# Kernel optimization log

Hardware: AMD Instinct MI355X
Metric: run time of the kernel (lower is better)

## Reference

```python
import jax, jax.numpy as jnp
import numpy as np

C, HEADS, H, W = 256, 8, 64, 64
HD = C // HEADS
EPS = 1e-5

def conv1x1(x, w, b):
    # x:[B,C,H,W], w:[O,C], b:[O]
    return jnp.einsum('bchw,oc->bohw', x, w) + b[None, :, None, None]

def group_norm(x, scale, bias):
    B = x.shape[0]
    xg = x.reshape(B, HEADS, HD, H, W)
    mu = jnp.mean(xg, axis=(2, 3, 4), keepdims=True)
    var = jnp.var(xg, axis=(2, 3, 4), keepdims=True)
    xn = ((xg - mu) * jax.lax.rsqrt(var + EPS)).reshape(B, C, H, W)
    return xn * scale[None, :, None, None] + bias[None, :, None, None]

def setup_inputs() -> dict:
    key = jax.random.key(0)
    ks = jax.random.split(key, 12)
    s = 1.0 / np.sqrt(C)
    d = {
        'x': jax.random.normal(ks[0], (1, C, H, W), jnp.float32),
        'wq': jax.random.normal(ks[1], (C, C), jnp.float32) * s,
        'bq': jax.random.normal(ks[2], (C,), jnp.float32) * 0.01,
        'wk': jax.random.normal(ks[3], (C, C), jnp.float32) * s,
        'bk': jax.random.normal(ks[4], (C,), jnp.float32) * 0.01,
        'wv': jax.random.normal(ks[5], (C, C), jnp.float32) * s,
        'bv': jax.random.normal(ks[6], (C,), jnp.float32) * 0.01,
        'wo': jax.random.normal(ks[7], (C, C), jnp.float32) * s,
        'bo': jax.random.normal(ks[8], (C,), jnp.float32) * 0.01,
        'gn_scale': jnp.ones((C,), jnp.float32),
        'gn_bias': jnp.zeros((C,), jnp.float32),
        'gamma': jax.random.normal(ks[9], (1,), jnp.float32) * 0.1,
    }
    return d

def reference(x, wq, bq, wk, bk, wv, bv, wo, bo, gn_scale, gn_bias, gamma):
    B = x.shape[0]
    N = H * W
    scale = HD ** (-0.5)
    xn = group_norm(x, gn_scale, gn_bias)
    q = conv1x1(xn, wq, bq).reshape(B, HEADS, HD, N)
    k = conv1x1(xn, wk, bk).reshape(B, HEADS, HD, N)
    v = conv1x1(xn, wv, bv).reshape(B, HEADS, HD, N)
    attn = jnp.einsum('bhdn,bhdm->bhnm', q, k) * scale  # [B,h,N,N]
    attn = jax.nn.softmax(attn, axis=-1)
    out = jnp.einsum('bhnm,bhdm->bhdn', attn, v).reshape(B, C, H, W)
    out = conv1x1(out, wo, bo)
    return x + gamma * out
```

## Files before the change

kernel.cpp:

```cpp
#include <hip/hip_runtime.h>
#include <hip/hip_bf16.h>

#define C_DIM 256
#define N_SP  4096
#define HEADS 8
#define HD    32
#define GSIZE (HD * N_SP)

typedef __attribute__((ext_vector_type(8))) short bf16x8;
typedef __attribute__((ext_vector_type(4))) float f32x4;
typedef __attribute__((ext_vector_type(4))) unsigned u32x4;

__device__ inline unsigned short f2bf(float f) {
  unsigned int u = __builtin_bit_cast(unsigned int, f);
  u = (u + 0x7fffu + ((u >> 16) & 1u)) >> 16;
  return (unsigned short)u;
}
__device__ inline float bf2f(unsigned short b) {
  return __builtin_bit_cast(float, (unsigned)b << 16);
}

__device__ inline unsigned cvtpk_bf16(float lo, float hi) {
  unsigned r;
  asm("v_cvt_pk_bf16_f32 %0, %1, %2" : "=v"(r) : "v"(lo), "v"(hi));
  return r;
}
__device__ inline void pl32swap(unsigned &x, unsigned &y) {
  asm("v_permlane32_swap_b32 %0, %1" : "+v"(x), "+v"(y));
}
__device__ inline void pl16swap(unsigned &x, unsigned &y) {
  asm("v_permlane16_swap_b32 %0, %1" : "+v"(x), "+v"(y));
}
__device__ inline void gload_lds16(const void* g, void* l) {
  __builtin_amdgcn_global_load_lds(
      (const __attribute__((address_space(1))) void*)g,
      (__attribute__((address_space(3))) void*)l, 16, 0, 0);
}

__global__ __launch_bounds__(1024) void stats_cvt(const float* __restrict__ x,
                                                  float* __restrict__ pstats,
                                                  const float* __restrict__ wq,
                                                  const float* __restrict__ wk,
                                                  const float* __restrict__ wv,
                                                  const float* __restrict__ wo,
                                                  unsigned short* __restrict__ dst) {
  int t = threadIdx.x;
  if (blockIdx.x < 64) {
    int g = blockIdx.x >> 3, sub = blockIdx.x & 7;
    const float4* xg = reinterpret_cast<const float4*>(
        x + (size_t)g * GSIZE + (size_t)sub * (GSIZE / 8));
    float s1 = 0.f, s2 = 0.f;
#pragma unroll
    for (int i = 0; i < 4; ++i) {
      float4 v = xg[t + i * 1024];
      s1 += v.x + v.y + v.z + v.w;
      s2 += v.x * v.x + v.y * v.y + v.z * v.z + v.w * v.w;
    }
    for (int off = 1; off < 64; off <<= 1) {
      s1 += __shfl_xor(s1, off);
      s2 += __shfl_xor(s2, off);
    }
    __shared__ float red[16][2];
    int wid = t >> 6;
    if ((t & 63) == 0) { red[wid][0] = s1; red[wid][1] = s2; }
    __syncthreads();
    if (t < 16) {
      s1 = red[t][0]; s2 = red[t][1];
      for (int off = 1; off < 16; off <<= 1) {
        s1 += __shfl_xor(s1, off);
        s2 += __shfl_xor(s2, off);
      }
      if (t == 0) {
        pstats[(g * 8 + sub) * 2] = s1;
        pstats[(g * 8 + sub) * 2 + 1] = s2;
      }
    }
  } else {
    int i = (blockIdx.x - 64) * 1024 + t;
    int mat = i >> 14;
    int idx = i & 16383;
    const float* src = (mat == 0) ? wq : (mat == 1) ? wk : (mat == 2) ? wv : wo;
    float4 v = reinterpret_cast<const float4*>(src)[idx];
    ushort4 o;
    o.x = f2bf(v.x); o.y = f2bf(v.y); o.z = f2bf(v.z); o.w = f2bf(v.w);
    reinterpret_cast<ushort4*>(dst + (size_t)mat * 65536)[idx] = o;
  }
}

__global__ __launch_bounds__(256) void gn_qkv(const float* __restrict__ x,
                                              const float* __restrict__ pstats,
                                              const float* __restrict__ gsc,
                                              const float* __restrict__ gbi,
                                              const unsigned short* __restrict__ wbf,
                                              const float* __restrict__ bq,
                                              const float* __restrict__ bk,
                                              const float* __restrict__ bv,
                                              unsigned short* __restrict__ qt,
                                              unsigned short* __restrict__ kt,
                                              unsigned short* __restrict__ vv) {
  __shared__ unsigned short xt[16][264];
  int t = threadIdx.x;
  int p0 = (blockIdx.x >> 1) * 16;
  int oh = (blockIdx.x & 1) * 128;

  {
    int pl = t & 15;
    int cb = t >> 4;
    int c0 = cb * 16;
    int g = c0 >> 5;
    float s1 = 0.f, s2 = 0.f;
#pragma unroll
    for (int s = 0; s < 8; ++s) {
      s1 += pstats[(g * 8 + s) * 2];
      s2 += pstats[(g * 8 + s) * 2 + 1];
    }
    float mu = s1 / (float)GSIZE;
    float rs = rsqrtf(s2 / (float)GSIZE - mu * mu + 1e-5f);
#pragma unroll
    for (int j = 0; j < 16; ++j) {
      float sc = gsc[c0 + j] * rs;
      float bi = gbi[c0 + j] - mu * sc;
      xt[pl][c0 + j] = f2bf(x[(size_t)(c0 + j) * N_SP + p0 + pl] * sc + bi);
    }
  }
  __syncthreads();

  int w = t >> 6, lc = t & 15, lg = (t & 63) >> 4;
  int ow = oh + w * 32;
  f32x4 aq[2], ak[2], av[2];
#pragma unroll
  for (int i = 0; i < 2; ++i) {
    aq[i] = (f32x4){0.f, 0.f, 0.f, 0.f};
    ak[i] = (f32x4){0.f, 0.f, 0.f, 0.f};
    av[i] = (f32x4){0.f, 0.f, 0.f, 0.f};
  }
#pragma unroll
  for (int it = 0; it < 8; ++it) {
    bf16x8 a = *reinterpret_cast<const bf16x8*>(&xt[lc][it * 32 + 8 * lg]);
#pragma unroll
    for (int ni = 0; ni < 2; ++ni) {
      size_t rowoff = (size_t)(ow + 16 * ni + lc) * C_DIM + it * 32 + 8 * lg;
      bf16x8 bQ = *reinterpret_cast<const bf16x8*>(wbf + rowoff);
      bf16x8 bK = *reinterpret_cast<const bf16x8*>(wbf + 65536 + rowoff);
      bf16x8 bV = *reinterpret_cast<const bf16x8*>(wbf + 131072 + rowoff);
      aq[ni] = __builtin_amdgcn_mfma_f32_16x16x32_bf16(a, bQ, aq[ni], 0, 0, 0);
      ak[ni] = __builtin_amdgcn_mfma_f32_16x16x32_bf16(a, bK, ak[ni], 0, 0, 0);
      av[ni] = __builtin_amdgcn_mfma_f32_16x16x32_bf16(bV, a, av[ni], 0, 0, 0);
    }
  }
#pragma unroll
  for (int ni = 0; ni < 2; ++ni) {
    int o = ow + 16 * ni + lc;
    float bqv = bq[o], bkv = bk[o];
#pragma unroll
    for (int r = 0; r < 4; ++r) {
      qt[(size_t)(p0 + 4 * lg + r) * C_DIM + o] =
          f2bf((aq[ni][r] + bqv) * 0.25503344494963116f);
      kt[(size_t)(p0 + 4 * lg + r) * C_DIM + o] = f2bf(ak[ni][r] + bkv);
    }
  }
#pragma unroll
  for (int mi = 0; mi < 2; ++mi)
#pragma unroll
    for (int r = 0; r < 4; ++r) {
      int o = ow + 16 * mi + 4 * lg + r;
      vv[(size_t)o * N_SP + p0 + lc] = f2bf(av[mi][r] + bv[o]);
    }
}


#define STAGE_Q(BB, IT)                                                       \
  {                                                                           \
    _Pragma("unroll")                                                         \
    for (int st = 0; st < 4; ++st) {                                          \
      gload_lds16(ksrc + (size_t)(IT) * 131072 + st * 32768,                  \
                  smem + (BB) + st * 4096 + w1024);                           \
      gload_lds16(vsrc + (size_t)(IT) * 512 + st * 128,                       \
                  smem + (BB) + 16384 + st * 4096 + w1024);                   \
    }                                                                         \
  }

#define CHAIN(KF, VF)                                                         \
  {                                                                           \
    f32x4 s[4];                                                               \
    _Pragma("unroll")                                                         \
    for (int ni = 0; ni < 4; ++ni) {                                          \
      f32x4 z = (f32x4){0.f, 0.f, 0.f, 0.f};                                  \
      s[ni] = __builtin_amdgcn_mfma_f32_16x16x32_bf16(KF[ni], qf[qi], z, 0, 0, 0); \
    }                                                                         \
    unsigned wd[4][2];                                                        \
    _Pragma("unroll")                                                         \
    for (int ni = 0; ni < 4; ++ni) {                                          \
      float p0e = __builtin_amdgcn_exp2f(s[ni][0]);                           \
      float p1e = __builtin_amdgcn_exp2f(s[ni][1]);                           \
      float p2e = __builtin_amdgcn_exp2f(s[ni][2]);                           \
      float p3e = __builtin_amdgcn_exp2f(s[ni][3]);                           \
      wd[ni][0] = cvtpk_bf16(p0e, p1e);                                       \
      wd[ni][1] = cvtpk_bf16(p2e, p3e);                                       \
    }                                                                         \
    bf16x8 ap[2];                                                             \
    _Pragma("unroll")                                                         \
    for (int kk = 0; kk < 2; ++kk) {                                          \
      unsigned a0 = wd[2 * kk][0], b0 = wd[2 * kk + 1][0];                    \
      unsigned a1 = wd[2 * kk][1], b1 = wd[2 * kk + 1][1];                    \
      pl32swap(a0, b0); pl16swap(a0, b0);                                     \
      pl32swap(a1, b1); pl16swap(a1, b1);                                     \
      u32x4 pk = {a0, a1, b0, b1};                                            \
      ap[kk] = __builtin_bit_cast(bf16x8, pk);                                \
    }                                                                         \
    lacc[qi] = __builtin_amdgcn_mfma_f32_16x16x32_bf16(ap[0], ones, lacc[qi], 0, 0, 0); \
    oacc[qi][0] = __builtin_amdgcn_mfma_f32_16x16x32_bf16(ap[0], VF[0][0], oacc[qi][0], 0, 0, 0); \
    oacc[qi][1] = __builtin_amdgcn_mfma_f32_16x16x32_bf16(ap[0], VF[0][1], oacc[qi][1], 0, 0, 0); \
    lacc[qi] = __builtin_amdgcn_mfma_f32_16x16x32_bf16(ap[1], ones, lacc[qi], 0, 0, 0); \
    oacc[qi][0] = __builtin_amdgcn_mfma_f32_16x16x32_bf16(ap[1], VF[1][0], oacc[qi][0], 0, 0, 0); \
    oacc[qi][1] = __builtin_amdgcn_mfma_f32_16x16x32_bf16(ap[1], VF[1][1], oacc[qi][1], 0, 0, 0); \
  }

#define COMPUTE_PAIR(BB, KOFF)                                                \
  {                                                                           \
    bf16x8 kf0[4], kf1[4], vf0[2][2], vf1[2][2];                              \
    _Pragma("unroll")                                                         \
    for (int ni = 0; ni < 4; ++ni) {                                          \
      kf0[ni] = *reinterpret_cast<const bf16x8*>(smem + (BB) + (KOFF) + ni * 1024 + krd); \
      kf1[ni] = *reinterpret_cast<const bf16x8*>(smem + (BB) + (KOFF) + 4096 + ni * 1024 + krd); \
    }                                                                         \
    _Pragma("unroll")                                                         \
    for (int dd = 0; dd < 2; ++dd) {                                          \
      vf0[0][dd] = *reinterpret_cast<const bf16x8*>(smem + (BB) + 16384 + (KOFF) + dd * 2048 + vrd0); \
      vf0[1][dd] = *reinterpret_cast<const bf16x8*>(smem + (BB) + 16384 + (KOFF) + dd * 2048 + vrd1); \
      vf1[0][dd] = *reinterpret_cast<const bf16x8*>(smem + (BB) + 16384 + (KOFF) + 4096 + dd * 2048 + vrd0); \
      vf1[1][dd] = *reinterpret_cast<const bf16x8*>(smem + (BB) + 16384 + (KOFF) + 4096 + dd * 2048 + vrd1); \
    }                                                                         \
    _Pragma("unroll")                                                         \
    for (int qi = 0; qi < 4; ++qi) {                                          \
      CHAIN(kf0, vf0)                                                         \
      CHAIN(kf1, vf1)                                                         \
    }                                                                         \
  }

#define SYNC_T                                                                \
  {                                                                           \
    asm volatile("s_waitcnt vmcnt(0)" ::: "memory");                          \
    __syncthreads();                                                          \
  }

__global__ __launch_bounds__(256, 2) void attn_part(const unsigned short* __restrict__ qt,
                                                    const unsigned short* __restrict__ kt,
                                                    const unsigned short* __restrict__ v,
                                                    unsigned short* __restrict__ po,
                                                    float* __restrict__ lp) {
  __shared__ __align__(1024) char smem[65536];
  int t = threadIdx.x;
  int w = t >> 6, lane = t & 63, lc = t & 15, lg = (t & 63) >> 4;
  int h = blockIdx.y, ks = blockIdx.z;
  int hc = h * HD;
  int nq0 = blockIdx.x * 256 + w * 64;
  int w1024 = w << 10;

  int kg = 64 * w + lane;
  int krow = kg >> 2;
  int kc16 = (kg & 3) ^ (krow & 3);
  const char* ksrc = (const char*)(kt + (size_t)(ks * 1024 + krow) * C_DIM + hc + 8 * kc16);
  int vg = 64 * w + lane;
  int vrow = vg >> 3;
  int vn16 = (vg & 7) ^ (vrow & 7);
  const char* vsrc = (const char*)(v + (size_t)(hc + vrow) * N_SP + ks * 1024 + 8 * vn16);

  int krd = lc * 64 + 16 * (lg ^ (lc & 3));
  int vrd0 = lc * 128 + 16 * ((lg + 0) ^ (lc & 7));
  int vrd1 = lc * 128 + 16 * ((lg + 4) ^ (lc & 7));

  bf16x8 qf[4];
#pragma unroll
  for (int qi = 0; qi < 4; ++qi)
    qf[qi] = *reinterpret_cast<const bf16x8*>(
        qt + (size_t)(nq0 + 16 * qi + lc) * C_DIM + hc + 8 * lg);

  f32x4 oacc[4][2], lacc[4];
#pragma unroll
  for (int qi = 0; qi < 4; ++qi) {
    lacc[qi] = (f32x4){0.f, 0.f, 0.f, 0.f};
#pragma unroll
    for (int dd = 0; dd < 2; ++dd) oacc[qi][dd] = (f32x4){0.f, 0.f, 0.f, 0.f};
  }
  const bf16x8 ones = {0x3F80, 0x3F80, 0x3F80, 0x3F80, 0x3F80, 0x3F80, 0x3F80, 0x3F80};

  STAGE_Q(0, 0)
  SYNC_T
  STAGE_Q(32768, 1)
  COMPUTE_PAIR(0, 0)
  COMPUTE_PAIR(0, 8192)
  SYNC_T
  STAGE_Q(0, 2)
  COMPUTE_PAIR(32768, 0)
  COMPUTE_PAIR(32768, 8192)
  SYNC_T
  STAGE_Q(32768, 3)
  COMPUTE_PAIR(0, 0)
  COMPUTE_PAIR(0, 8192)
  SYNC_T
  COMPUTE_PAIR(32768, 0)
  COMPUTE_PAIR(32768, 8192)

  unsigned short* pob = po + (size_t)ks * (N_SP * C_DIM);
#pragma unroll
  for (int qi = 0; qi < 4; ++qi)
#pragma unroll
    for (int dd = 0; dd < 2; ++dd)
#pragma unroll
      for (int r = 0; r < 4; ++r)
        pob[(size_t)(nq0 + 16 * qi + 4 * lg + r) * C_DIM + hc + 16 * dd + lc] =
            f2bf(oacc[qi][dd][r]);
  if (lc == 0) {
#pragma unroll
    for (int qi = 0; qi < 4; ++qi)
#pragma unroll
      for (int r = 0; r < 4; ++r)
        lp[ks * 32768 + h * N_SP + nq0 + 16 * qi + 4 * lg + r] = lacc[qi][r];
  }
}

__global__ __launch_bounds__(256) void attn_merge(const unsigned short* __restrict__ po,
                                                  const float* __restrict__ lp,
                                                  unsigned short* __restrict__ aot) {
  int i = blockIdx.x * 256 + threadIdx.x;
  int n = i >> 5;
  int c0 = (i & 31) * 8;
  int h = c0 >> 5;
  float l = lp[h * N_SP + n] + lp[32768 + h * N_SP + n] +
            lp[65536 + h * N_SP + n] + lp[98304 + h * N_SP + n];
  float rl = 1.0f / l;
  float acc[8] = {0.f, 0.f, 0.f, 0.f, 0.f, 0.f, 0.f, 0.f};
#pragma unroll
  for (int ksplit = 0; ksplit < 4; ++ksplit) {
    bf16x8 vv = *reinterpret_cast<const bf16x8*>(po + (size_t)ksplit * (N_SP * C_DIM) + (size_t)i * 8);
#pragma unroll
    for (int j = 0; j < 8; ++j) acc[j] += bf2f((unsigned short)vv[j]);
  }
  bf16x8 o;
#pragma unroll
  for (int j = 0; j < 8; ++j) o[j] = (short)f2bf(acc[j] * rl);
  *reinterpret_cast<bf16x8*>(aot + (size_t)i * 8) = o;
}

__global__ __launch_bounds__(256) void gemm_out(const unsigned short* __restrict__ Wb,
                                                const unsigned short* __restrict__ aot,
                                                const float* __restrict__ bias,
                                                const float* __restrict__ x,
                                                const float* __restrict__ gamma,
                                                float* __restrict__ out) {
  int t = threadIdx.x;
  int w = t >> 6, lc = t & 15, lg = (t & 63) >> 4;
  int o_base = blockIdx.y * 64 + (w >> 1) * 32;
  int p_base = blockIdx.x * 64 + (w & 1) * 32;
  f32x4 acc[2][2];
#pragma unroll
  for (int mi = 0; mi < 2; ++mi)
#pragma unroll
    for (int ni = 0; ni < 2; ++ni) acc[mi][ni] = (f32x4){0.f, 0.f, 0.f, 0.f};
#pragma unroll
  for (int c0 = 0; c0 < 256; c0 += 32) {
    bf16x8 a[2], b[2];
#pragma unroll
    for (int mi = 0; mi < 2; ++mi)
      a[mi] = *reinterpret_cast<const bf16x8*>(
          Wb + (size_t)(o_base + 16 * mi + lc) * C_DIM + c0 + 8 * lg);
#pragma unroll
    for (int ni = 0; ni < 2; ++ni)
      b[ni] = *reinterpret_cast<const bf16x8*>(
          aot + (size_t)(p_base + 16 * ni + lc) * C_DIM + c0 + 8 * lg);
#pragma unroll
    for (int mi = 0; mi < 2; ++mi)
#pragma unroll
      for (int ni = 0; ni < 2; ++ni)
        acc[mi][ni] = __builtin_amdgcn_mfma_f32_16x16x32_bf16(a[mi], b[ni], acc[mi][ni], 0, 0, 0);
  }
  float g = gamma[0];
#pragma unroll
  for (int mi = 0; mi < 2; ++mi)
#pragma unroll
    for (int r = 0; r < 4; ++r) {
      int o = o_base + 16 * mi + 4 * lg + r;
      float bvv = bias[o];
#pragma unroll
      for (int ni = 0; ni < 2; ++ni) {
        size_t idx = (size_t)o * N_SP + p_base + 16 * ni + lc;
        out[idx] = x[idx] + g * (acc[mi][ni][r] + bvv);
      }
    }
}

extern "C" void kernel_launch(void* const* d_in, const int* in_sizes, int n_in,
                              void* d_out, int out_size, void* d_ws, size_t ws_size,
                              hipStream_t stream) {
  const float* x   = (const float*)d_in[0];
  const float* wq  = (const float*)d_in[1];
  const float* bq  = (const float*)d_in[2];
  const float* wk  = (const float*)d_in[3];
  const float* bk  = (const float*)d_in[4];
  const float* wv  = (const float*)d_in[5];
  const float* bv  = (const float*)d_in[6];
  const float* wo  = (const float*)d_in[7];
  const float* bo  = (const float*)d_in[8];
  const float* gsc = (const float*)d_in[9];
  const float* gbi = (const float*)d_in[10];
  const float* gamma = (const float*)d_in[11];
  float* out = (float*)d_out;

  char* ws = (char*)d_ws;
  float* pstats         = (float*)(ws + 256);
  unsigned short* wbf   = (unsigned short*)(ws + 1024);
  unsigned short* qt    = (unsigned short*)(ws + 525312);
  unsigned short* kt    = (unsigned short*)(ws + 2622464);
  unsigned short* vv    = (unsigned short*)(ws + 4719616);
  unsigned short* aot   = (unsigned short*)(ws + 6816768);
  float* lp             = (float*)(ws + 8913920);
  unsigned short* po    = (unsigned short*)(ws + 12059648);

  stats_cvt<<<128, 1024, 0, stream>>>(x, pstats, wq, wk, wv, wo, wbf);
  gn_qkv<<<512, 256, 0, stream>>>(x, pstats, gsc, gbi, wbf, bq, bk, bv, qt, kt, vv);
  attn_part<<<dim3(16, 8, 4), 256, 0, stream>>>(qt, kt, vv, po, lp);
  attn_merge<<<512, 256, 0, stream>>>(po, lp, aot);
  gemm_out<<<dim3(64, 4), 256, 0, stream>>>(wbf + 3 * 65536, aot, bo, x, gamma, out);
}
```

Before: 63.72 us.

## Split attention keys eight ways with smaller LDS stages for more blocks

Doubles the key-split factor of the partial attention kernel from 4 to 8, so each block handles 512 keys instead of 1024. The LDS stage is halved to 32 KB, and launch bounds now request 4 blocks per CU, which gives 1024 blocks and more occupancy to hide latency. In exchange the merge kernel reads and sums twice as many bf16 partial outputs and denominators, which adds global memory traffic. Workspace use for the po and lp partials also doubles.

```diff
diff --git a/kernel.cpp b/kernel.cpp
--- a/kernel.cpp
+++ b/kernel.cpp
@@ -169,15 +169,12 @@
 }
 
 
-#define STAGE_Q(BB, IT)                                                       \
+#define STAGE_P(BB, IT)                                                       \
   {                                                                           \
-    _Pragma("unroll")                                                         \
-    for (int st = 0; st < 4; ++st) {                                          \
-      gload_lds16(ksrc + (size_t)(IT) * 131072 + st * 32768,                  \
-                  smem + (BB) + st * 4096 + w1024);                           \
-      gload_lds16(vsrc + (size_t)(IT) * 512 + st * 128,                       \
-                  smem + (BB) + 16384 + st * 4096 + w1024);                   \
-    }                                                                         \
+    gload_lds16(ksrc + (size_t)(IT) * 65536, smem + (BB) + w1024);            \
+    gload_lds16(ksrc + (size_t)(IT) * 65536 + 32768, smem + (BB) + 4096 + w1024); \
+    gload_lds16(vsrc + (size_t)(IT) * 256, smem + (BB) + 8192 + w1024);       \
+    gload_lds16(vsrc + (size_t)(IT) * 256 + 128, smem + (BB) + 12288 + w1024);\
   }
 
 #define CHAIN(KF, VF)                                                         \
@@ -216,20 +213,20 @@
     oacc[qi][1] = __builtin_amdgcn_mfma_f32_16x16x32_bf16(ap[1], VF[1][1], oacc[qi][1], 0, 0, 0); \
   }
 
-#define COMPUTE_PAIR(BB, KOFF)                                                \
+#define COMPUTE_P(BB)                                                         \
   {                                                                           \
     bf16x8 kf0[4], kf1[4], vf0[2][2], vf1[2][2];                              \
     _Pragma("unroll")                                                         \
     for (int ni = 0; ni < 4; ++ni) {                                          \
-      kf0[ni] = *reinterpret_cast<const bf16x8*>(smem + (BB) + (KOFF) + ni * 1024 + krd); \
-      kf1[ni] = *reinterpret_cast<const bf16x8*>(smem + (BB) + (KOFF) + 4096 + ni * 1024 + krd); \
+      kf0[ni] = *reinterpret_cast<const bf16x8*>(smem + (BB) + ni * 1024 + krd); \
+      kf1[ni] = *reinterpret_cast<const bf16x8*>(smem + (BB) + 4096 + ni * 1024 + krd); \
     }                                                                         \
     _Pragma("unroll")                                                         \
     for (int dd = 0; dd < 2; ++dd) {                                          \
-      vf0[0][dd] = *reinterpret_cast<const bf16x8*>(smem + (BB) + 16384 + (KOFF) + dd * 2048 + vrd0); \
-      vf0[1][dd] = *reinterpret_cast<const bf16x8*>(smem + (BB) + 16384 + (KOFF) + dd * 2048 + vrd1); \
-      vf1[0][dd] = *reinterpret_cast<const bf16x8*>(smem + (BB) + 16384 + (KOFF) + 4096 + dd * 2048 + vrd0); \
-      vf1[1][dd] = *reinterpret_cast<const bf16x8*>(smem + (BB) + 16384 + (KOFF) + 4096 + dd * 2048 + vrd1); \
+      vf0[0][dd] = *reinterpret_cast<const bf16x8*>(smem + (BB) + 8192 + dd * 2048 + vrd0); \
+      vf0[1][dd] = *reinterpret_cast<const bf16x8*>(smem + (BB) + 8192 + dd * 2048 + vrd1); \
+      vf1[0][dd] = *reinterpret_cast<const bf16x8*>(smem + (BB) + 12288 + dd * 2048 + vrd0); \
+      vf1[1][dd] = *reinterpret_cast<const bf16x8*>(smem + (BB) + 12288 + dd * 2048 + vrd1); \
     }                                                                         \
     _Pragma("unroll")                                                         \
     for (int qi = 0; qi < 4; ++qi) {                                          \
@@ -244,12 +241,12 @@
     __syncthreads();                                                          \
   }
 
-__global__ __launch_bounds__(256, 2) void attn_part(const unsigned short* __restrict__ qt,
+__global__ __launch_bounds__(256, 4) void attn_part(const unsigned short* __restrict__ qt,
                                                     const unsigned short* __restrict__ kt,
                                                     const unsigned short* __restrict__ v,
                                                     unsigned short* __restrict__ po,
                                                     float* __restrict__ lp) {
-  __shared__ __align__(1024) char smem[65536];
+  __shared__ __align__(1024) char smem[32768];
   int t = threadIdx.x;
   int w = t >> 6, lane = t & 63, lc = t & 15, lg = (t & 63) >> 4;
   int h = blockIdx.y, ks = blockIdx.z;
@@ -260,11 +257,11 @@
   int kg = 64 * w + lane;
   int krow = kg >> 2;
   int kc16 = (kg & 3) ^ (krow & 3);
-  const char* ksrc = (const char*)(kt + (size_t)(ks * 1024 + krow) * C_DIM + hc + 8 * kc16);
+  const char* ksrc = (const char*)(kt + (size_t)(ks * 512 + krow) * C_DIM + hc + 8 * kc16);
   int vg = 64 * w + lane;
   int vrow = vg >> 3;
   int vn16 = (vg & 7) ^ (vrow & 7);
-  const char* vsrc = (const char*)(v + (size_t)(hc + vrow) * N_SP + ks * 1024 + 8 * vn16);
+  const char* vsrc = (const char*)(v + (size_t)(hc + vrow) * N_SP + ks * 512 + 8 * vn16);
 
   int krd = lc * 64 + 16 * (lg ^ (lc & 3));
   int vrd0 = lc * 128 + 16 * ((lg + 0) ^ (lc & 7));
@@ -285,22 +282,18 @@
   }
   const bf16x8 ones = {0x3F80, 0x3F80, 0x3F80, 0x3F80, 0x3F80, 0x3F80, 0x3F80, 0x3F80};
 
-  STAGE_Q(0, 0)
+  STAGE_P(0, 0)
   SYNC_T
-  STAGE_Q(32768, 1)
-  COMPUTE_PAIR(0, 0)
-  COMPUTE_PAIR(0, 8192)
+  STAGE_P(16384, 1)
+  COMPUTE_P(0)
   SYNC_T
-  STAGE_Q(0, 2)
-  COMPUTE_PAIR(32768, 0)
-  COMPUTE_PAIR(32768, 8192)
+  STAGE_P(0, 2)
+  COMPUTE_P(16384)
   SYNC_T
-  STAGE_Q(32768, 3)
-  COMPUTE_PAIR(0, 0)
-  COMPUTE_PAIR(0, 8192)
+  STAGE_P(16384, 3)
+  COMPUTE_P(0)
   SYNC_T
-  COMPUTE_PAIR(32768, 0)
-  COMPUTE_PAIR(32768, 8192)
+  COMPUTE_P(16384)
 
   unsigned short* pob = po + (size_t)ks * (N_SP * C_DIM);
 #pragma unroll
@@ -327,12 +320,14 @@
   int n = i >> 5;
   int c0 = (i & 31) * 8;
   int h = c0 >> 5;
-  float l = lp[h * N_SP + n] + lp[32768 + h * N_SP + n] +
-            lp[65536 + h * N_SP + n] + lp[98304 + h * N_SP + n];
+  float l = 0.f;
+#pragma unroll
+  for (int ksplit = 0; ksplit < 8; ++ksplit)
+    l += lp[ksplit * 32768 + h * N_SP + n];
   float rl = 1.0f / l;
   float acc[8] = {0.f, 0.f, 0.f, 0.f, 0.f, 0.f, 0.f, 0.f};
 #pragma unroll
-  for (int ksplit = 0; ksplit < 4; ++ksplit) {
+  for (int ksplit = 0; ksplit < 8; ++ksplit) {
     bf16x8 vv = *reinterpret_cast<const bf16x8*>(po + (size_t)ksplit * (N_SP * C_DIM) + (size_t)i * 8);
 #pragma unroll
     for (int j = 0; j < 8; ++j) acc[j] += bf2f((unsigned short)vv[j]);
@@ -419,7 +414,7 @@
 
   stats_cvt<<<128, 1024, 0, stream>>>(x, pstats, wq, wk, wv, wo, wbf);
   gn_qkv<<<512, 256, 0, stream>>>(x, pstats, gsc, gbi, wbf, bq, bk, bv, qt, kt, vv);
-  attn_part<<<dim3(16, 8, 4), 256, 0, stream>>>(qt, kt, vv, po, lp);
+  attn_part<<<dim3(16, 8, 8), 256, 0, stream>>>(qt, kt, vv, po, lp);
   attn_merge<<<512, 256, 0, stream>>>(po, lp, aot);
   gemm_out<<<dim3(64, 4), 256, 0, stream>>>(wbf + 3 * 65536, aot, bo, x, gamma, out);
 }
```

Result: slower. 93.34 us (+46.5%).

## Split keys across warps within block and merge in LDS, dropping merge kernel

Applied to the files above, without the earlier changes.

Attention is restructured so each block handles 64 queries of one head, and its four warps each sweep a separate quarter of the keys. Each warp double-buffers its own private LDS region, so there are no block-wide barriers in the main loop. Partial outputs and row sums are reduced through LDS at the end and normalised in-kernel. This removes the global partial buffers, the separate attn_merge launch and the per-stage __syncthreads. The trade-off is that each block streams more K/V per query and the per-warp stages are smaller, which may lower memory efficiency.

```diff
diff --git a/kernel.cpp b/kernel.cpp
--- a/kernel.cpp
+++ b/kernel.cpp
@@ -169,15 +169,16 @@
 }
 
 
-#define STAGE_Q(BB, IT)                                                       \
+#define STAGE_W(BUF, IT)                                                      \
   {                                                                           \
     _Pragma("unroll")                                                         \
-    for (int st = 0; st < 4; ++st) {                                          \
-      gload_lds16(ksrc + (size_t)(IT) * 131072 + st * 32768,                  \
-                  smem + (BB) + st * 4096 + w1024);                           \
-      gload_lds16(vsrc + (size_t)(IT) * 512 + st * 128,                       \
-                  smem + (BB) + 16384 + st * 4096 + w1024);                   \
-    }                                                                         \
+    for (int i = 0; i < 4; ++i)                                               \
+      gload_lds16(ksrc + (size_t)(IT) * 32768 + i * 8192,                     \
+                  region + (BUF) * 8192 + i * 1024);                          \
+    _Pragma("unroll")                                                         \
+    for (int j = 0; j < 4; ++j)                                               \
+      gload_lds16(vsrc + (size_t)(IT) * 128 + j * 65536,                      \
+                  region + (BUF) * 8192 + 4096 + j * 1024);                   \
   }
 
 #define CHAIN(KF, VF)                                                         \
@@ -216,55 +217,50 @@
     oacc[qi][1] = __builtin_amdgcn_mfma_f32_16x16x32_bf16(ap[1], VF[1][1], oacc[qi][1], 0, 0, 0); \
   }
 
-#define COMPUTE_PAIR(BB, KOFF)                                                \
+#define COMPUTE_W(BUF)                                                        \
   {                                                                           \
-    bf16x8 kf0[4], kf1[4], vf0[2][2], vf1[2][2];                              \
-    _Pragma("unroll")                                                         \
-    for (int ni = 0; ni < 4; ++ni) {                                          \
-      kf0[ni] = *reinterpret_cast<const bf16x8*>(smem + (BB) + (KOFF) + ni * 1024 + krd); \
-      kf1[ni] = *reinterpret_cast<const bf16x8*>(smem + (BB) + (KOFF) + 4096 + ni * 1024 + krd); \
+    bf16x8 kf[4], vf[2][2];                                                   \
+    _Pragma("unroll")                                                         \
+    for (int ni = 0; ni < 4; ++ni)                                            \
+      kf[ni] = *reinterpret_cast<const bf16x8*>(region + (BUF) * 8192 + ni * 1024 + krd); \
+    _Pragma("unroll")                                                         \
+    for (int dd = 0; dd < 2; ++dd) {                                          \
+      vf[0][dd] = *reinterpret_cast<const bf16x8*>(region + (BUF) * 8192 + 4096 + dd * 2048 + vrd0); \
+      vf[1][dd] = *reinterpret_cast<const bf16x8*>(region + (BUF) * 8192 + 4096 + dd * 2048 + vrd1); \
     }                                                                         \
     _Pragma("unroll")                                                         \
-    for (int dd = 0; dd < 2; ++dd) {                                          \
-      vf0[0][dd] = *reinterpret_cast<const bf16x8*>(smem + (BB) + 16384 + (KOFF) + dd * 2048 + vrd0); \
-      vf0[1][dd] = *reinterpret_cast<const bf16x8*>(smem + (BB) + 16384 + (KOFF) + dd * 2048 + vrd1); \
-      vf1[0][dd] = *reinterpret_cast<const bf16x8*>(smem + (BB) + 16384 + (KOFF) + 4096 + dd * 2048 + vrd0); \
-      vf1[1][dd] = *reinterpret_cast<const bf16x8*>(smem + (BB) + 16384 + (KOFF) + 4096 + dd * 2048 + vrd1); \
-    }                                                                         \
-    _Pragma("unroll")                                                         \
-    for (int qi = 0; qi < 4; ++qi) {                                          \
-      CHAIN(kf0, vf0)                                                         \
-      CHAIN(kf1, vf1)                                                         \
-    }                                                                         \
-  }
-
-#define SYNC_T                                                                \
+    for (int qi = 0; qi < 4; ++qi) { CHAIN(kf, vf) }                          \
+  }
+
+#define WAIT_VM(N)                                                            \
   {                                                                           \
-    asm volatile("s_waitcnt vmcnt(0)" ::: "memory");                          \
-    __syncthreads();                                                          \
+    asm volatile("s_waitcnt vmcnt(" #N ")" ::: "memory");                     \
+    __builtin_amdgcn_sched_barrier(0);                                        \
+  }
+#define WAIT_LGKM                                                             \
+  {                                                                           \
+    asm volatile("s_waitcnt lgkmcnt(0)" ::: "memory");                        \
+    __builtin_amdgcn_sched_barrier(0);                                        \
   }
 
 __global__ __launch_bounds__(256, 2) void attn_part(const unsigned short* __restrict__ qt,
                                                     const unsigned short* __restrict__ kt,
                                                     const unsigned short* __restrict__ v,
-                                                    unsigned short* __restrict__ po,
-                                                    float* __restrict__ lp) {
+                                                    unsigned short* __restrict__ aot) {
   __shared__ __align__(1024) char smem[65536];
   int t = threadIdx.x;
   int w = t >> 6, lane = t & 63, lc = t & 15, lg = (t & 63) >> 4;
-  int h = blockIdx.y, ks = blockIdx.z;
+  int h = blockIdx.y;
   int hc = h * HD;
-  int nq0 = blockIdx.x * 256 + w * 64;
-  int w1024 = w << 10;
-
-  int kg = 64 * w + lane;
-  int krow = kg >> 2;
-  int kc16 = (kg & 3) ^ (krow & 3);
-  const char* ksrc = (const char*)(kt + (size_t)(ks * 1024 + krow) * C_DIM + hc + 8 * kc16);
-  int vg = 64 * w + lane;
-  int vrow = vg >> 3;
-  int vn16 = (vg & 7) ^ (vrow & 7);
-  const char* vsrc = (const char*)(v + (size_t)(hc + vrow) * N_SP + ks * 1024 + 8 * vn16);
+  int nq0 = blockIdx.x * 64;
+  char* region = smem + w * 16384;
+
+  int krow = lane >> 2;
+  int kc16 = (lane & 3) ^ (krow & 3);
+  const char* ksrc = (const char*)(kt + (size_t)(w * 1024 + krow) * C_DIM + hc + 8 * kc16);
+  int vrow = lane >> 3;
+  int vn16 = (lane & 7) ^ (vrow & 7);
+  const char* vsrc = (const char*)(v + (size_t)(hc + vrow) * N_SP + w * 1024 + 8 * vn16);
 
   int krd = lc * 64 + 16 * (lg ^ (lc & 3));
   int vrd0 = lc * 128 + 16 * ((lg + 0) ^ (lc & 7));
@@ -285,62 +281,47 @@
   }
   const bf16x8 ones = {0x3F80, 0x3F80, 0x3F80, 0x3F80, 0x3F80, 0x3F80, 0x3F80, 0x3F80};
 
-  STAGE_Q(0, 0)
-  SYNC_T
-  STAGE_Q(32768, 1)
-  COMPUTE_PAIR(0, 0)
-  COMPUTE_PAIR(0, 8192)
-  SYNC_T
-  STAGE_Q(0, 2)
-  COMPUTE_PAIR(32768, 0)
-  COMPUTE_PAIR(32768, 8192)
-  SYNC_T
-  STAGE_Q(32768, 3)
-  COMPUTE_PAIR(0, 0)
-  COMPUTE_PAIR(0, 8192)
-  SYNC_T
-  COMPUTE_PAIR(32768, 0)
-  COMPUTE_PAIR(32768, 8192)
-
-  unsigned short* pob = po + (size_t)ks * (N_SP * C_DIM);
-#pragma unroll
-  for (int qi = 0; qi < 4; ++qi)
+  STAGE_W(0, 0)
+  STAGE_W(1, 1)
+#pragma unroll 1
+  for (int it = 0; it < 14; ++it) {
+    WAIT_VM(8)
+    COMPUTE_W(it & 1)
+    WAIT_LGKM
+    STAGE_W(it & 1, it + 2)
+  }
+  WAIT_VM(8)
+  COMPUTE_W(0)
+  WAIT_VM(0)
+  COMPUTE_W(1)
+
+#pragma unroll
+  for (int qi = 0; qi < 4; ++qi) {
 #pragma unroll
     for (int dd = 0; dd < 2; ++dd)
-#pragma unroll
-      for (int r = 0; r < 4; ++r)
-        pob[(size_t)(nq0 + 16 * qi + 4 * lg + r) * C_DIM + hc + 16 * dd + lc] =
-            f2bf(oacc[qi][dd][r]);
-  if (lc == 0) {
-#pragma unroll
-    for (int qi = 0; qi < 4; ++qi)
-#pragma unroll
-      for (int r = 0; r < 4; ++r)
-        lp[ks * 32768 + h * N_SP + nq0 + 16 * qi + 4 * lg + r] = lacc[qi][r];
-  }
-}
-
-__global__ __launch_bounds__(256) void attn_merge(const unsigned short* __restrict__ po,
-                                                  const float* __restrict__ lp,
-                                                  unsigned short* __restrict__ aot) {
-  int i = blockIdx.x * 256 + threadIdx.x;
-  int n = i >> 5;
-  int c0 = (i & 31) * 8;
-  int h = c0 >> 5;
-  float l = lp[h * N_SP + n] + lp[32768 + h * N_SP + n] +
-            lp[65536 + h * N_SP + n] + lp[98304 + h * N_SP + n];
-  float rl = 1.0f / l;
-  float acc[8] = {0.f, 0.f, 0.f, 0.f, 0.f, 0.f, 0.f, 0.f};
-#pragma unroll
-  for (int ksplit = 0; ksplit < 4; ++ksplit) {
-    bf16x8 vv = *reinterpret_cast<const bf16x8*>(po + (size_t)ksplit * (N_SP * C_DIM) + (size_t)i * 8);
-#pragma unroll
-    for (int j = 0; j < 8; ++j) acc[j] += bf2f((unsigned short)vv[j]);
-  }
-  bf16x8 o;
-#pragma unroll
-  for (int j = 0; j < 8; ++j) o[j] = (short)f2bf(acc[j] * rl);
-  *reinterpret_cast<bf16x8*>(aot + (size_t)i * 8) = o;
+      *reinterpret_cast<f32x4*>(region + (((qi * 3 + dd) * 64) + lane) * 16) = oacc[qi][dd];
+    *reinterpret_cast<f32x4*>(region + (((qi * 3 + 2) * 64) + lane) * 16) = lacc[qi];
+  }
+  __syncthreads();
+  f32x4 osum[2], lsum;
+  osum[0] = (f32x4){0.f, 0.f, 0.f, 0.f};
+  osum[1] = (f32x4){0.f, 0.f, 0.f, 0.f};
+  lsum = (f32x4){0.f, 0.f, 0.f, 0.f};
+#pragma unroll
+  for (int wp = 0; wp < 4; ++wp) {
+    const char* rr = smem + wp * 16384;
+    osum[0] += *reinterpret_cast<const f32x4*>(rr + (((w * 3 + 0) * 64) + lane) * 16);
+    osum[1] += *reinterpret_cast<const f32x4*>(rr + (((w * 3 + 1) * 64) + lane) * 16);
+    lsum += *reinterpret_cast<const f32x4*>(rr + (((w * 3 + 2) * 64) + lane) * 16);
+  }
+#pragma unroll
+  for (int r = 0; r < 4; ++r) {
+    float rl = 1.0f / lsum[r];
+#pragma unroll
+    for (int dd = 0; dd < 2; ++dd)
+      aot[(size_t)(nq0 + 16 * w + 4 * lg + r) * C_DIM + hc + 16 * dd + lc] =
+          f2bf(osum[dd][r] * rl);
+  }
 }
 
 __global__ __launch_bounds__(256) void gemm_out(const unsigned short* __restrict__ Wb,
@@ -414,12 +395,9 @@
   unsigned short* kt    = (unsigned short*)(ws + 2622464);
   unsigned short* vv    = (unsigned short*)(ws + 4719616);
   unsigned short* aot   = (unsigned short*)(ws + 6816768);
-  float* lp             = (float*)(ws + 8913920);
-  unsigned short* po    = (unsigned short*)(ws + 12059648);
 
   stats_cvt<<<128, 1024, 0, stream>>>(x, pstats, wq, wk, wv, wo, wbf);
   gn_qkv<<<512, 256, 0, stream>>>(x, pstats, gsc, gbi, wbf, bq, bk, bv, qt, kt, vv);
-  attn_part<<<dim3(16, 8, 4), 256, 0, stream>>>(qt, kt, vv, po, lp);
-  attn_merge<<<512, 256, 0, stream>>>(po, lp, aot);
+  attn_part<<<dim3(64, 8), 256, 0, stream>>>(qt, kt, vv, aot);
   gemm_out<<<dim3(64, 4), 256, 0, stream>>>(wbf + 3 * 65536, aot, bo, x, gamma, out);
 }
```

Measured after the change: 61.74 us, median of 2. 3.1% less time.
